# Kernel tuning notes

Hardware: AMD Instinct MI355X
Metric: run time of the kernel (lower is better)

## Reference

```python
import jax, jax.numpy as jnp
import numpy as np

N = 50000       # num vertices
E_SEG = 80000   # num hyperedges
NNZ = 400000    # incidence pairs
FIN = 512       # input feature dim
H = 256         # MLP_hidden
C = 40          # num classes
NLAYER = 2      # All_num_layers
ALPHA = 0.5     # restart_alpha


def _w(k, shape):
    return jax.random.normal(k, shape, jnp.float32) * (1.0 / np.sqrt(shape[0]))


def setup_inputs() -> dict:
    key = jax.random.key(0)
    ks = jax.random.split(key, 12)
    return {
        "x": jax.random.normal(ks[0], (N, FIN), jnp.float32),
        "vertex": jax.random.randint(ks[1], (NNZ,), 0, N),
        "edges": jax.random.randint(ks[2], (NNZ,), 0, E_SEG),
        "lin_in_w": _w(ks[3], (FIN, H)), "lin_in_b": jnp.zeros((H,), jnp.float32),
        "w1": _w(ks[4], (H, H)),   "b1": jnp.zeros((H,), jnp.float32),
        "w2": _w(ks[5], (2 * H, H)), "b2": jnp.zeros((H,), jnp.float32),
        "w3": _w(ks[6], (H, H)),   "b3": jnp.zeros((H,), jnp.float32),
        "cls_w1": _w(ks[7], (H, H)), "cls_b1": jnp.zeros((H,), jnp.float32),
        "cls_w2": _w(ks[8], (H, C)), "cls_b2": jnp.zeros((C,), jnp.float32),
    }


def reference(x, vertex, edges, lin_in_w, lin_in_b, w1, b1, w2, b2, w3, b3,
              cls_w1, cls_b1, cls_w2, cls_b2):
    # input projection (dropout is identity at p=0)
    x = jax.nn.relu(x @ lin_in_w + lin_in_b)           # [N, H]
    x0 = x
    for _ in range(NLAYER):  # same conv weights reused each layer
        # W1 (1-layer MLP = Linear), gather to incidences
        xve = (x @ w1 + b1)[vertex]                    # [NNZ, H]
        # scatter-add to hyperedges
        xe = jax.ops.segment_sum(xve, edges, num_segments=E_SEG)  # [E, H]
        # gather back, concat with vertex feats, W2 (Linear on 2H)
        xev = jnp.concatenate([x[vertex], xe[edges]], axis=-1) @ w2 + b2  # [NNZ, H]
        # scatter-add to vertices
        xv = jax.ops.segment_sum(xev, vertex, num_segments=N)     # [N, H]
        # restart connection + W (Linear) + outer activation
        x = (1.0 - ALPHA) * xv + ALPHA * x0
        x = jax.nn.relu(x @ w3 + b3)
    # classifier MLP (2 layers: Linear -> relu -> Linear)
    h = jax.nn.relu(x @ cls_w1 + cls_b1)
    return h @ cls_w2 + cls_b2                          # [N, C]
```

## Files before the change

kernel.cpp:

```cpp
#include <hip/hip_runtime.h>
#include <hip/hip_bf16.h>
#include <cstdint>
#include <cstddef>

#define HD   256
#define NV   50000
#define NE   80000
#define NNZC 400000
#define FINC 512
#define NCLS 40

using bf16 = __hip_bfloat16;

typedef short bf16x8v __attribute__((ext_vector_type(8)));
typedef float f32x4   __attribute__((ext_vector_type(4)));

#define NCH_E ((NE + 1023) / 1024)
#define NCH_V ((NV + 1023) / 1024)

__device__ __forceinline__ float b2f(unsigned short u) {
    union { unsigned int i; float f; } c; c.i = ((unsigned int)u) << 16; return c.f;
}
__device__ __forceinline__ unsigned short f2b(float f) {
    union { float f; unsigned int i; } c; c.f = f;
    return (unsigned short)((c.i + 0x7FFFu + ((c.i >> 16) & 1u)) >> 16);
}
__device__ __forceinline__ float4 load4f(const bf16* p) {
    ushort4 u = *reinterpret_cast<const ushort4*>(p);
    return make_float4(b2f(u.x), b2f(u.y), b2f(u.z), b2f(u.w));
}
__device__ __forceinline__ void store4(bf16* p, float4 v) {
    ushort4 u; u.x = f2b(v.x); u.y = f2b(v.y); u.z = f2b(v.z); u.w = f2b(v.w);
    *reinterpret_cast<ushort4*>(p) = u;
}

__device__ __forceinline__ void gl_lds16(const bf16* g, short* l) {
    __builtin_amdgcn_global_load_lds(
        (const __attribute__((address_space(1))) unsigned int*)g,
        (__attribute__((address_space(3))) unsigned int*)l,
        16, 0, 0);
}

__global__ __launch_bounds__(256)
void fill0_k(unsigned int* __restrict__ p, long long n)
{
    long long i = (long long)blockIdx.x * 256 + threadIdx.x;
    long long stride = (long long)gridDim.x * 256;
    for (; i < n; i += stride) p[i] = 0u;
}

__global__ __launch_bounds__(256)
void hist_k(const int* __restrict__ vertex, const int* __restrict__ edges,
            int* __restrict__ cnt_v, int* __restrict__ cnt_e, int nnz)
{
    int i = blockIdx.x * 256 + threadIdx.x;
    if (i < nnz) {
        atomicAdd(&cnt_v[vertex[i]], 1);
        atomicAdd(&cnt_e[edges[i]], 1);
    }
}

__global__ __launch_bounds__(256)
void scan_part2_k(const int* __restrict__ cnt_e, int* __restrict__ off_e, int* __restrict__ part_e,
                  const int* __restrict__ cnt_v, int* __restrict__ off_v, int* __restrict__ part_v)
{
    const int* cnt; int* off; int* part; int n;
    if (blockIdx.y == 0) { cnt = cnt_e; off = off_e; part = part_e; n = NE; }
    else                 { cnt = cnt_v; off = off_v; part = part_v; n = NV; }
    int base = blockIdx.x * 1024;
    if (base >= n) return;
    __shared__ int s[256];
    int idx = base + threadIdx.x * 4;
    int v[4], sum = 0;
    #pragma unroll
    for (int j = 0; j < 4; ++j) { v[j] = (idx + j < n) ? cnt[idx + j] : 0; sum += v[j]; }
    s[threadIdx.x] = sum;
    __syncthreads();
    #pragma unroll
    for (int d = 1; d < 256; d <<= 1) {
        int t = (threadIdx.x >= d) ? s[threadIdx.x - d] : 0;
        __syncthreads();
        s[threadIdx.x] += t;
        __syncthreads();
    }
    int excl = s[threadIdx.x] - sum;
    #pragma unroll
    for (int j = 0; j < 4; ++j) {
        if (idx + j < n) off[idx + j] = excl;
        excl += v[j];
    }
    if (threadIdx.x == 255) part[blockIdx.x] = s[255];
}

__global__ __launch_bounds__(256)
void scan_top2_k(int* __restrict__ part_e, int* __restrict__ end_e,
                 int* __restrict__ part_v, int* __restrict__ end_v)
{
    int* part; int* endp; int nch;
    if (blockIdx.x == 0) { part = part_e; endp = end_e; nch = NCH_E; }
    else                 { part = part_v; endp = end_v; nch = NCH_V; }
    __shared__ int s[256];
    int v = (threadIdx.x < nch) ? part[threadIdx.x] : 0;
    s[threadIdx.x] = v;
    __syncthreads();
    #pragma unroll
    for (int d = 1; d < 256; d <<= 1) {
        int t = (threadIdx.x >= d) ? s[threadIdx.x - d] : 0;
        __syncthreads();
        s[threadIdx.x] += t;
        __syncthreads();
    }
    if (threadIdx.x < nch) part[threadIdx.x] = s[threadIdx.x] - v;
    if (threadIdx.x == 255) *endp = s[255];
}

__global__ __launch_bounds__(256)
void scan_addcur2_k(int* __restrict__ off_e, const int* __restrict__ part_e, int* __restrict__ cur_e,
                    int* __restrict__ off_v, const int* __restrict__ part_v, int* __restrict__ cur_v)
{
    int n; int* off; const int* part; int* cur;
    if (blockIdx.y == 0) { n = NE; off = off_e; part = part_e; cur = cur_e; }
    else                 { n = NV; off = off_v; part = part_v; cur = cur_v; }
    int i = blockIdx.x * 256 + threadIdx.x;
    if (i < n) { int o = off[i] + part[i >> 10]; off[i] = o; cur[i] = o; }
}

__global__ __launch_bounds__(256)
void csr_fill_k(const int* __restrict__ vertex, const int* __restrict__ edges,
                int* __restrict__ cur_e, int* __restrict__ cur_v,
                int* __restrict__ adj_e, int* __restrict__ adj_v, int nnz)
{
    int i = blockIdx.x * 256 + threadIdx.x;
    if (i >= nnz) return;
    int v = vertex[i], e = edges[i];
    adj_e[atomicAdd(&cur_e[e], 1)] = v;
    adj_v[atomicAdd(&cur_v[v], 1)] = e;
}

__global__ __launch_bounds__(256)
void prep_w_k(const float* __restrict__ lin_w, const float* __restrict__ w1,
              const float* __restrict__ w2, const float* __restrict__ w3,
              const float* __restrict__ cw1, const float* __restrict__ cw2,
              const float* __restrict__ b2,
              unsigned short* __restrict__ lin_wt, unsigned short* __restrict__ w1t,
              unsigned short* __restrict__ w2a_nb, unsigned short* __restrict__ w2b_nb,
              unsigned short* __restrict__ w3t, unsigned short* __restrict__ cw1t,
              unsigned short* __restrict__ cw2t, float* __restrict__ b2w3)
{
    int idx = blockIdx.x * 256 + threadIdx.x;
    if (idx < 131072) { int n = idx >> 9, k = idx & 511; lin_wt[idx] = f2b(lin_w[k * 256 + n]); return; }
    idx -= 131072;
    if (idx < 65536) { int n = idx >> 8, k = idx & 255; w1t[idx] = f2b(w1[k * 256 + n]); return; }
    idx -= 65536;
    if (idx < 65536) { w2a_nb[idx] = f2b(w2[idx]); return; }
    idx -= 65536;
    if (idx < 65536) { w2b_nb[idx] = f2b(w2[65536 + idx]); return; }
    idx -= 65536;
    if (idx < 65536) { int n = idx >> 8, k = idx & 255; w3t[idx] = f2b(w3[k * 256 + n]); return; }
    idx -= 65536;
    if (idx < 65536) { int n = idx >> 8, k = idx & 255; cw1t[idx] = f2b(cw1[k * 256 + n]); return; }
    idx -= 65536;
    if (idx < 12288) { int n = idx >> 8, k = idx & 255; cw2t[idx] = f2b((n < NCLS) ? cw2[k * NCLS + n] : 0.f); return; }
    idx -= 12288;
    if (idx < 256) {
        float s = 0.f;
        for (int k = 0; k < 256; ++k) s += b2[k] * w3[k * 256 + idx];
        b2w3[idx] = s;
    }
}

__global__ __launch_bounds__(256)
void xcvt_k(const float* __restrict__ x, unsigned short* __restrict__ o, long long n4)
{
    long long i = (long long)blockIdx.x * 256 + threadIdx.x;
    long long stride = (long long)gridDim.x * 256;
    for (; i < n4; i += stride) {
        float4 v = reinterpret_cast<const float4*>(x)[i];
        ushort4 u; u.x = f2b(v.x); u.y = f2b(v.y); u.z = f2b(v.z); u.w = f2b(v.w);
        reinterpret_cast<ushort4*>(o)[i] = u;
    }
}

template<int EPI>
__global__ __launch_bounds__(256)
void mgemm_k(const bf16* __restrict__ Ag, const bf16* __restrict__ Bt,
             const float* __restrict__ bias, const float* __restrict__ bias2,
             const int* __restrict__ deg,
             const bf16* __restrict__ Sb, const bf16* __restrict__ z0b,
             const float* __restrict__ b2w3v,
             bf16* __restrict__ Cg, bf16* __restrict__ Cg2,
             int M, int K, int Nc)
{
    __shared__ __align__(16) short As[128 * 64];
    __shared__ __align__(16) short Bs[128 * 64];

    const int t  = threadIdx.x;
    const int wv = t >> 6, l = t & 63;
    const int wr = wv >> 1, wc = wv & 1;
    const int bn = blockIdx.x * 128;
    const int bm = blockIdx.y * 128;
    const int l15 = l & 15;

    f32x4 acc[4][4];
    #pragma unroll
    for (int m = 0; m < 4; ++m)
        #pragma unroll
        for (int n = 0; n < 4; ++n)
            acc[m][n] = (f32x4){0.f, 0.f, 0.f, 0.f};

    const int brow8 = l >> 3;
    const int bcol  = (l & 7) * 8;

    for (int k0 = 0; k0 < K; k0 += 64) {
        #pragma unroll
        for (int i = 0; i < 4; ++i) {
            int c = wv * 4 + i;
            int row = c * 8 + brow8;
            int ga = bm + row; if (ga >= M) ga = M - 1;
            gl_lds16(Ag + (size_t)ga * K + k0 + bcol, As + c * 512);
        }
        #pragma unroll
        for (int i = 0; i < 4; ++i) {
            int c = wv * 4 + i;
            int row = c * 8 + brow8;
            gl_lds16(Bt + (size_t)(bn + row) * K + k0 + bcol, Bs + c * 512);
        }
        __syncthreads();

        #pragma unroll
        for (int ks = 0; ks < 2; ++ks) {
            bf16x8v a[4], b[4];
            const int kb = ks * 64 + (l >> 4) * 16;
            #pragma unroll
            for (int m = 0; m < 4; ++m) {
                int r = wr * 64 + m * 16 + l15;
                a[m] = *reinterpret_cast<const bf16x8v*>((const char*)As + r * 128 + kb);
            }
            #pragma unroll
            for (int n = 0; n < 4; ++n) {
                int r = wc * 64 + n * 16 + l15;
                b[n] = *reinterpret_cast<const bf16x8v*>((const char*)Bs + r * 128 + kb);
            }
            #pragma unroll
            for (int m = 0; m < 4; ++m)
                #pragma unroll
                for (int n = 0; n < 4; ++n)
                    acc[m][n] = __builtin_amdgcn_mfma_f32_16x16x32_bf16(a[m], b[n], acc[m][n], 0, 0, 0);
        }
        __syncthreads();
    }

    if (EPI == 3) {
        bool second = (bn >= 256);
        bf16* CC = second ? Cg2 : Cg;
        const float* bb = second ? bias2 : bias;
        int cb = bn - (second ? 256 : 0);
        float bv[4];
        #pragma unroll
        for (int n = 0; n < 4; ++n)
            bv[n] = bb ? bb[cb + wc * 64 + n * 16 + l15] : 0.f;
        #pragma unroll
        for (int m = 0; m < 4; ++m) {
            #pragma unroll
            for (int i = 0; i < 4; ++i) {
                int row = bm + wr * 64 + m * 16 + (l >> 4) * 4 + i;
                if (row >= M) continue;
                size_t base = (size_t)row * 256 + cb + wc * 64 + l15;
                #pragma unroll
                for (int n = 0; n < 4; ++n)
                    reinterpret_cast<unsigned short*>(CC)[base + n * 16] = f2b(acc[m][n][i] + bv[n]);
            }
        }
    } else if (EPI == 4) {
        float bv[4], bw[4];
        #pragma unroll
        for (int n = 0; n < 4; ++n) {
            int col = bn + wc * 64 + n * 16 + l15;
            bv[n] = bias[col];
            bw[n] = b2w3v[col];
        }
        #pragma unroll
        for (int m = 0; m < 4; ++m) {
            #pragma unroll
            for (int i = 0; i < 4; ++i) {
                int row = bm + wr * 64 + m * 16 + (l >> 4) * 4 + i;
                if (row >= M) continue;
                float d = (float)deg[row];
                size_t base = (size_t)row * Nc + bn + wc * 64 + l15;
                #pragma unroll
                for (int n = 0; n < 4; ++n) {
                    size_t idx = base + (size_t)n * 16;
                    float sv = b2f(reinterpret_cast<const unsigned short*>(Sb)[idx]);
                    float zv = b2f(reinterpret_cast<const unsigned short*>(z0b)[idx]);
                    float v = 0.5f * (d * (sv + bw[n]) + acc[m][n][i]) + 0.5f * zv + bv[n];
                    v = fmaxf(v, 0.f);
                    reinterpret_cast<unsigned short*>(Cg)[idx] = f2b(v);
                }
            }
        }
    } else {
        float bv[4];
        #pragma unroll
        for (int n = 0; n < 4; ++n)
            bv[n] = bias ? bias[bn + wc * 64 + n * 16 + l15] : 0.f;
        #pragma unroll
        for (int m = 0; m < 4; ++m) {
            #pragma unroll
            for (int i = 0; i < 4; ++i) {
                int row = bm + wr * 64 + m * 16 + (l >> 4) * 4 + i;
                if (row >= M) continue;
                size_t base = (size_t)row * Nc + bn + wc * 64 + l15;
                #pragma unroll
                for (int n = 0; n < 4; ++n) {
                    float v = acc[m][n][i] + bv[n];
                    if (EPI == 1) v = fmaxf(v, 0.f);
                    reinterpret_cast<unsigned short*>(Cg)[base + n * 16] = f2b(v);
                }
            }
        }
    }
}

__global__ __launch_bounds__(256)
void gather_sum_k(const bf16* __restrict__ src, const int* __restrict__ adj,
                  const int* __restrict__ off, bf16* __restrict__ dst, int nseg)
{
    int seg = blockIdx.x * 4 + (threadIdx.x >> 6);
    if (seg >= nseg) return;
    int lane = threadIdx.x & 63;
    int s0 = off[seg], s1 = off[seg + 1];
    float4 acc = make_float4(0.f, 0.f, 0.f, 0.f);
    int j = s0;
    for (; j + 2 <= s1; j += 2) {
        int r0 = adj[j], r1 = adj[j + 1];
        float4 v0 = load4f(src + (size_t)r0 * HD + lane * 4);
        float4 v1 = load4f(src + (size_t)r1 * HD + lane * 4);
        acc.x += v0.x + v1.x; acc.y += v0.y + v1.y;
        acc.z += v0.z + v1.z; acc.w += v0.w + v1.w;
    }
    if (j < s1) {
        float4 v = load4f(src + (size_t)adj[j] * HD + lane * 4);
        acc.x += v.x; acc.y += v.y; acc.z += v.z; acc.w += v.w;
    }
    store4(dst + (size_t)seg * HD + lane * 4, acc);
}

__global__ __launch_bounds__(256)
void cls_mfma_k(const bf16* __restrict__ Hm, const bf16* __restrict__ Wt,
                const float* __restrict__ bias, float* __restrict__ out, int M)
{
    const int wv = threadIdx.x >> 6, l = threadIdx.x & 63;
    const int l15 = l & 15;
    const int r0 = blockIdx.x * 64 + wv * 16;
    f32x4 acc[3];
    #pragma unroll
    for (int n = 0; n < 3; ++n) acc[n] = (f32x4){0.f, 0.f, 0.f, 0.f};

    int arow = r0 + l15; if (arow >= M) arow = M - 1;
    const int ko = (l >> 4) * 8;
    for (int kk = 0; kk < HD; kk += 32) {
        bf16x8v a = *reinterpret_cast<const bf16x8v*>(Hm + (size_t)arow * HD + kk + ko);
        #pragma unroll
        for (int n = 0; n < 3; ++n) {
            bf16x8v b = *reinterpret_cast<const bf16x8v*>(Wt + (size_t)(n * 16 + l15) * HD + kk + ko);
            acc[n] = __builtin_amdgcn_mfma_f32_16x16x32_bf16(a, b, acc[n], 0, 0, 0);
        }
    }
    #pragma unroll
    for (int n = 0; n < 3; ++n) {
        int col = n * 16 + l15;
        if (col >= NCLS) continue;
        float bv = bias[col];
        #pragma unroll
        for (int i = 0; i < 4; ++i) {
            int row = r0 + (l >> 4) * 4 + i;
            if (row < M) out[(size_t)row * NCLS + col] = acc[n][i] + bv;
        }
    }
}

extern "C" void kernel_launch(void* const* d_in, const int* in_sizes, int n_in,
                              void* d_out, int out_size, void* d_ws, size_t ws_size,
                              hipStream_t stream)
{
    const float* x_in   = (const float*)d_in[0];
    const int*   vertex = (const int*)d_in[1];
    const int*   edges  = (const int*)d_in[2];
    const float* lin_w  = (const float*)d_in[3];
    const float* lin_b  = (const float*)d_in[4];
    const float* w1     = (const float*)d_in[5];
    const float* b1     = (const float*)d_in[6];
    const float* w2     = (const float*)d_in[7];
    const float* b2     = (const float*)d_in[8];
    const float* w3     = (const float*)d_in[9];
    const float* b3     = (const float*)d_in[10];
    const float* cw1    = (const float*)d_in[11];
    const float* cb1    = (const float*)d_in[12];
    const float* cw2    = (const float*)d_in[13];
    const float* cb2    = (const float*)d_in[14];
    float* out = (float*)d_out;
    (void)in_sizes; (void)n_in; (void)out_size; (void)ws_size;

    char* ws = (char*)d_ws;
    const size_t nvhd = (size_t)NV * HD, nehd = (size_t)NE * HD;
    size_t off = 0;
    auto alloc = [&](size_t bytes) { char* p = ws + off; off += (bytes + 255) & ~(size_t)255; return p; };
    bf16* x0 = (bf16*)alloc(nvhd * 2);
    bf16* xA = (bf16*)alloc(nvhd * 2);
    bf16* E1 = (bf16*)alloc(nehd * 2);
    bf16* E2 = (bf16*)alloc(nehd * 2);
    bf16* xf = (bf16*)alloc((size_t)NV * FINC * 2);
    bf16* S  = xf;
    bf16* z0 = xf + nvhd;
    unsigned short* lin_wt = (unsigned short*)alloc(256 * 512 * 2);
    unsigned short* w1t    = (unsigned short*)alloc(256 * 256 * 2);
    unsigned short* W23at  = (unsigned short*)alloc(256 * 256 * 2);
    unsigned short* W23bt  = (unsigned short*)alloc(256 * 256 * 2);
    unsigned short* w2ab   = (unsigned short*)alloc(512 * 256 * 2);
    unsigned short* w2a_nb = w2ab;
    unsigned short* w2b_nb = w2ab + 256 * 256;
    unsigned short* w3t    = (unsigned short*)alloc(256 * 256 * 2);
    unsigned short* cw1t   = (unsigned short*)alloc(256 * 256 * 2);
    unsigned short* cw2t   = (unsigned short*)alloc(48 * 256 * 2);
    float* b2w3 = (float*)alloc(256 * 4);
    int* cnt_e = (int*)alloc(NE * 4);
    int* cnt_v = (int*)alloc(NV * 4);
    int* off_e = (int*)alloc((NE + 1) * 4);
    int* off_v = (int*)alloc((NV + 1) * 4);
    int* cur_e = (int*)alloc(NE * 4);
    int* cur_v = (int*)alloc(NV * 4);
    int* part_e = (int*)alloc(256 * 4);
    int* part_v = (int*)alloc(256 * 4);
    int* adj_e = (int*)alloc((size_t)NNZC * 4);
    int* adj_v = (int*)alloc((size_t)NNZC * 4);

    dim3 blk(256);
    dim3 gv(2, (NV + 127) / 128);
    dim3 gv4(4, (NV + 127) / 128);
    dim3 gin(2, (NV + 127) / 128);
    dim3 gw(4, 2);

    fill0_k<<<128, blk, 0, stream>>>((unsigned int*)cnt_e, NE + NV);
    hist_k<<<(NNZC + 255) / 256, blk, 0, stream>>>(vertex, edges, cnt_v, cnt_e, NNZC);
    scan_part2_k<<<dim3(NCH_E, 2), blk, 0, stream>>>(cnt_e, off_e, part_e, cnt_v, off_v, part_v);
    scan_top2_k<<<2, blk, 0, stream>>>(part_e, off_e + NE, part_v, off_v + NV);
    scan_addcur2_k<<<dim3((NE + 255) / 256, 2), blk, 0, stream>>>(off_e, part_e, cur_e,
                                                                  off_v, part_v, cur_v);
    csr_fill_k<<<(NNZC + 255) / 256, blk, 0, stream>>>(vertex, edges, cur_e, cur_v, adj_e, adj_v, NNZC);

    prep_w_k<<<1841, blk, 0, stream>>>(lin_w, w1, w2, w3, cw1, cw2, b2,
                                       lin_wt, w1t, w2a_nb, w2b_nb, w3t, cw1t, cw2t, b2w3);
    mgemm_k<3><<<gw, blk, 0, stream>>>((const bf16*)w3t, (const bf16*)w2ab,
        nullptr, nullptr, nullptr, nullptr, nullptr, nullptr,
        (bf16*)W23at, (bf16*)W23bt, 256, 256, 512);

    xcvt_k<<<2048, blk, 0, stream>>>(x_in, (unsigned short*)xf, (long long)NV * FINC / 4);
    mgemm_k<1><<<gin, blk, 0, stream>>>(xf, (const bf16*)lin_wt,
        lin_b, nullptr, nullptr, nullptr, nullptr, nullptr,
        x0, nullptr, NV, FINC, HD);
    mgemm_k<0><<<gv, blk, 0, stream>>>(x0, (const bf16*)w3t,
        nullptr, nullptr, nullptr, nullptr, nullptr, nullptr,
        z0, nullptr, NV, HD, HD);

    const bf16* cur = x0;
    for (int layer = 0; layer < 2; ++layer) {
        mgemm_k<3><<<gv4, blk, 0, stream>>>(cur, (const bf16*)w1t,
            b1, nullptr, nullptr, nullptr, nullptr, nullptr,
            E1, S, NV, HD, 512);
        gather_sum_k<<<(NE + 3) / 4, blk, 0, stream>>>(E1, adj_e, off_e, E2, NE);
        gather_sum_k<<<(NV + 3) / 4, blk, 0, stream>>>(E2, adj_v, off_v, E1, NV);
        mgemm_k<4><<<gv, blk, 0, stream>>>(E1, (const bf16*)W23bt,
            b3, nullptr, cnt_v, S, z0, b2w3,
            xA, nullptr, NV, HD, HD);
        cur = xA;
    }

    mgemm_k<1><<<gv, blk, 0, stream>>>(xA, (const bf16*)cw1t,
        cb1, nullptr, nullptr, nullptr, nullptr, nullptr,
        E1, nullptr, NV, HD, HD);
    cls_mfma_k<<<(NV + 63) / 64, blk, 0, stream>>>(E1, (const bf16*)cw2t, cb2, out, NV);
}
```

Measured before the change: 542.4 us.

## Fuse fp32 input conversion into GEMM, merge z0 GEMM, unroll gather by four

```diff
diff --git a/kernel.cpp b/kernel.cpp
--- a/kernel.cpp
+++ b/kernel.cpp
@@ -169,26 +169,14 @@
     }
 }
 
-__global__ __launch_bounds__(256)
-void xcvt_k(const float* __restrict__ x, unsigned short* __restrict__ o, long long n4)
-{
-    long long i = (long long)blockIdx.x * 256 + threadIdx.x;
-    long long stride = (long long)gridDim.x * 256;
-    for (; i < n4; i += stride) {
-        float4 v = reinterpret_cast<const float4*>(x)[i];
-        ushort4 u; u.x = f2b(v.x); u.y = f2b(v.y); u.z = f2b(v.z); u.w = f2b(v.w);
-        reinterpret_cast<ushort4*>(o)[i] = u;
-    }
-}
-
-template<int EPI>
-__global__ __launch_bounds__(256)
-void mgemm_k(const bf16* __restrict__ Ag, const bf16* __restrict__ Bt,
+template<int EPI, bool AF32>
+__global__ __launch_bounds__(256)
+void mgemm_k(const void* __restrict__ Agv, const bf16* __restrict__ Bt,
              const float* __restrict__ bias, const float* __restrict__ bias2,
              const int* __restrict__ deg,
              const bf16* __restrict__ Sb, const bf16* __restrict__ z0b,
              const float* __restrict__ b2w3v,
-             bf16* __restrict__ Cg, bf16* __restrict__ Cg2,
+             bf16* __restrict__ Cg, bf16* __restrict__ Cg2, bf16* __restrict__ Cg3,
              int M, int K, int Nc)
 {
     __shared__ __align__(16) short As[128 * 64];
@@ -212,12 +200,33 @@
     const int bcol  = (l & 7) * 8;
 
     for (int k0 = 0; k0 < K; k0 += 64) {
-        #pragma unroll
-        for (int i = 0; i < 4; ++i) {
-            int c = wv * 4 + i;
-            int row = c * 8 + brow8;
-            int ga = bm + row; if (ga >= M) ga = M - 1;
-            gl_lds16(Ag + (size_t)ga * K + k0 + bcol, As + c * 512);
+        if constexpr (AF32) {
+            const float* Af = (const float*)Agv;
+            #pragma unroll
+            for (int p = 0; p < 4; ++p) {
+                int idx8 = p * 256 + t;
+                int row  = idx8 >> 3;
+                int cg   = (idx8 & 7) * 8;
+                int ga = bm + row; if (ga >= M) ga = M - 1;
+                const float* src = Af + (size_t)ga * K + k0 + cg;
+                f32x4 u = *reinterpret_cast<const f32x4*>(src);
+                f32x4 v = *reinterpret_cast<const f32x4*>(src + 4);
+                bf16x8v o;
+                o[0] = (short)f2b(u[0]); o[1] = (short)f2b(u[1]);
+                o[2] = (short)f2b(u[2]); o[3] = (short)f2b(u[3]);
+                o[4] = (short)f2b(v[0]); o[5] = (short)f2b(v[1]);
+                o[6] = (short)f2b(v[2]); o[7] = (short)f2b(v[3]);
+                *reinterpret_cast<bf16x8v*>(As + row * 64 + cg) = o;
+            }
+        } else {
+            const bf16* Ab = (const bf16*)Agv;
+            #pragma unroll
+            for (int i = 0; i < 4; ++i) {
+                int c = wv * 4 + i;
+                int row = c * 8 + brow8;
+                int ga = bm + row; if (ga >= M) ga = M - 1;
+                gl_lds16(Ab + (size_t)ga * K + k0 + bcol, As + c * 512);
+            }
         }
         #pragma unroll
         for (int i = 0; i < 4; ++i) {
@@ -251,10 +260,10 @@
     }
 
     if (EPI == 3) {
-        bool second = (bn >= 256);
-        bf16* CC = second ? Cg2 : Cg;
-        const float* bb = second ? bias2 : bias;
-        int cb = bn - (second ? 256 : 0);
+        int oi = bn >> 8;
+        bf16* CC = (oi == 0) ? Cg : (oi == 1) ? Cg2 : Cg3;
+        const float* bb = (oi == 0) ? bias : (oi == 1) ? bias2 : nullptr;
+        int cb = bn & 255;
         float bv[4];
         #pragma unroll
         for (int n = 0; n < 4; ++n)
@@ -331,14 +340,18 @@
     int s0 = off[seg], s1 = off[seg + 1];
     float4 acc = make_float4(0.f, 0.f, 0.f, 0.f);
     int j = s0;
-    for (; j + 2 <= s1; j += 2) {
-        int r0 = adj[j], r1 = adj[j + 1];
+    for (; j + 4 <= s1; j += 4) {
+        int r0 = adj[j], r1 = adj[j + 1], r2 = adj[j + 2], r3 = adj[j + 3];
         float4 v0 = load4f(src + (size_t)r0 * HD + lane * 4);
         float4 v1 = load4f(src + (size_t)r1 * HD + lane * 4);
-        acc.x += v0.x + v1.x; acc.y += v0.y + v1.y;
-        acc.z += v0.z + v1.z; acc.w += v0.w + v1.w;
-    }
-    if (j < s1) {
+        float4 v2 = load4f(src + (size_t)r2 * HD + lane * 4);
+        float4 v3 = load4f(src + (size_t)r3 * HD + lane * 4);
+        acc.x += (v0.x + v1.x) + (v2.x + v3.x);
+        acc.y += (v0.y + v1.y) + (v2.y + v3.y);
+        acc.z += (v0.z + v1.z) + (v2.z + v3.z);
+        acc.w += (v0.w + v1.w) + (v2.w + v3.w);
+    }
+    for (; j < s1; ++j) {
         float4 v = load4f(src + (size_t)adj[j] * HD + lane * 4);
         acc.x += v.x; acc.y += v.y; acc.z += v.z; acc.w += v.w;
     }
@@ -409,17 +422,16 @@
     bf16* xA = (bf16*)alloc(nvhd * 2);
     bf16* E1 = (bf16*)alloc(nehd * 2);
     bf16* E2 = (bf16*)alloc(nehd * 2);
-    bf16* xf = (bf16*)alloc((size_t)NV * FINC * 2);
-    bf16* S  = xf;
-    bf16* z0 = xf + nvhd;
-    unsigned short* lin_wt = (unsigned short*)alloc(256 * 512 * 2);
-    unsigned short* w1t    = (unsigned short*)alloc(256 * 256 * 2);
-    unsigned short* W23at  = (unsigned short*)alloc(256 * 256 * 2);
+    bf16* S  = (bf16*)alloc(nvhd * 2);
+    bf16* z0 = (bf16*)alloc(nvhd * 2);
+    unsigned short* w1t    = (unsigned short*)alloc(3 * 256 * 256 * 2);
+    unsigned short* W23at  = w1t + 65536;
+    unsigned short* w3t    = w1t + 131072;
     unsigned short* W23bt  = (unsigned short*)alloc(256 * 256 * 2);
     unsigned short* w2ab   = (unsigned short*)alloc(512 * 256 * 2);
     unsigned short* w2a_nb = w2ab;
     unsigned short* w2b_nb = w2ab + 256 * 256;
-    unsigned short* w3t    = (unsigned short*)alloc(256 * 256 * 2);
+    unsigned short* lin_wt = (unsigned short*)alloc(256 * 512 * 2);
     unsigned short* cw1t   = (unsigned short*)alloc(256 * 256 * 2);
     unsigned short* cw2t   = (unsigned short*)alloc(48 * 256 * 2);
     float* b2w3 = (float*)alloc(256 * 4);
@@ -437,7 +449,7 @@
     dim3 blk(256);
     dim3 gv(2, (NV + 127) / 128);
     dim3 gv4(4, (NV + 127) / 128);
-    dim3 gin(2, (NV + 127) / 128);
+    dim3 gv6(6, (NV + 127) / 128);
     dim3 gw(4, 2);
 
     fill0_k<<<128, blk, 0, stream>>>((unsigned int*)cnt_e, NE + NV);
@@ -450,33 +462,35 @@
 
     prep_w_k<<<1841, blk, 0, stream>>>(lin_w, w1, w2, w3, cw1, cw2, b2,
                                        lin_wt, w1t, w2a_nb, w2b_nb, w3t, cw1t, cw2t, b2w3);
-    mgemm_k<3><<<gw, blk, 0, stream>>>((const bf16*)w3t, (const bf16*)w2ab,
+    mgemm_k<3, false><<<gw, blk, 0, stream>>>((const bf16*)w3t, (const bf16*)w2ab,
         nullptr, nullptr, nullptr, nullptr, nullptr, nullptr,
-        (bf16*)W23at, (bf16*)W23bt, 256, 256, 512);
-
-    xcvt_k<<<2048, blk, 0, stream>>>(x_in, (unsigned short*)xf, (long long)NV * FINC / 4);
-    mgemm_k<1><<<gin, blk, 0, stream>>>(xf, (const bf16*)lin_wt,
+        (bf16*)W23at, (bf16*)W23bt, nullptr, 256, 256, 512);
+
+    mgemm_k<1, true><<<gv, blk, 0, stream>>>(x_in, (const bf16*)lin_wt,
         lin_b, nullptr, nullptr, nullptr, nullptr, nullptr,
-        x0, nullptr, NV, FINC, HD);
-    mgemm_k<0><<<gv, blk, 0, stream>>>(x0, (const bf16*)w3t,
-        nullptr, nullptr, nullptr, nullptr, nullptr, nullptr,
-        z0, nullptr, NV, HD, HD);
+        x0, nullptr, nullptr, NV, FINC, HD);
 
     const bf16* cur = x0;
     for (int layer = 0; layer < 2; ++layer) {
-        mgemm_k<3><<<gv4, blk, 0, stream>>>(cur, (const bf16*)w1t,
-            b1, nullptr, nullptr, nullptr, nullptr, nullptr,
-            E1, S, NV, HD, 512);
+        if (layer == 0) {
+            mgemm_k<3, false><<<gv6, blk, 0, stream>>>(cur, (const bf16*)w1t,
+                b1, nullptr, nullptr, nullptr, nullptr, nullptr,
+                E1, S, z0, NV, HD, 768);
+        } else {
+            mgemm_k<3, false><<<gv4, blk, 0, stream>>>(cur, (const bf16*)w1t,
+                b1, nullptr, nullptr, nullptr, nullptr, nullptr,
+                E1, S, nullptr, NV, HD, 512);
+        }
         gather_sum_k<<<(NE + 3) / 4, blk, 0, stream>>>(E1, adj_e, off_e, E2, NE);
         gather_sum_k<<<(NV + 3) / 4, blk, 0, stream>>>(E2, adj_v, off_v, E1, NV);
-        mgemm_k<4><<<gv, blk, 0, stream>>>(E1, (const bf16*)W23bt,
+        mgemm_k<4, false><<<gv, blk, 0, stream>>>(E1, (const bf16*)W23bt,
             b3, nullptr, cnt_v, S, z0, b2w3,
-            xA, nullptr, NV, HD, HD);
+            xA, nullptr, nullptr, NV, HD, HD);
         cur = xA;
     }
 
-    mgemm_k<1><<<gv, blk, 0, stream>>>(xA, (const bf16*)cw1t,
+    mgemm_k<1, false><<<gv, blk, 0, stream>>>(xA, (const bf16*)cw1t,
         cb1, nullptr, nullptr, nullptr, nullptr, nullptr,
-        E1, nullptr, NV, HD, HD);
+        E1, nullptr, nullptr, NV, HD, HD);
     cls_mfma_k<<<(NV + 63) / 64, blk, 0, stream>>>(E1, (const bf16*)cw2t, cb2, out, NV);
 }
```

Measured after the change: 510.4 us. -5.9%, faster.
